# Performance work log

Hardware: AMD Instinct MI355X
Metric: run time of the kernel (lower is better)

Reference implementation:

```python
import jax, jax.numpy as jnp
import numpy as np

TAU = 2.0        # LIF membrane time constant
V_TH = 1.0       # spike threshold (spikingjelly default)
ALPHA = 4.0      # surrogate.Sigmoid default alpha
T_STEPS = 4
NUM_HEADS = 8


@jax.custom_vjp
def spike(x):
    # Heaviside(x) with sigmoid surrogate gradient (x = v - v_threshold)
    return (x >= 0.0).astype(x.dtype)

def _spike_fwd(x):
    return spike(x), x

def _spike_bwd(x, g):
    sg = jax.nn.sigmoid(ALPHA * x)
    return (g * ALPHA * sg * (1.0 - sg),)

spike.defvjp(_spike_fwd, _spike_bwd)


def multistep_lif(x_seq):
    """MultiStepLIFNode(tau=2, v_reset=0, detach_reset=True), x_seq: [T, ...]."""
    def step(v, x):
        v = v + (x - v) / TAU                     # decay_input=True charge
        s = spike(v - V_TH)
        v = v * (1.0 - jax.lax.stop_gradient(s))  # hard reset, detached
        return v, s
    _, s_seq = jax.lax.scan(step, jnp.zeros_like(x_seq[0]), x_seq)
    return s_seq


def setup_inputs() -> dict:
    key = jax.random.key(0)
    kx, kq, kk, kv = jax.random.split(key, 4)
    B, S, C = 2, 1024, 512
    scale = 1.0 / np.sqrt(C)
    return {
        "x": jax.random.normal(kx, (B, S, C), dtype=jnp.float32),
        "Wq": jax.random.normal(kq, (C, C), dtype=jnp.float32) * scale,
        "Wk": jax.random.normal(kk, (C, C), dtype=jnp.float32) * scale,
        "Wv": jax.random.normal(kv, (C, C), dtype=jnp.float32) * scale,
    }


def reference(x, Wq, Wk, Wv):
    B, S, C = x.shape
    H = NUM_HEADS
    hd = C // H
    # replicate input over T timesteps: [T, B, S, C]
    xt = jnp.broadcast_to(x[None], (T_STEPS, B, S, C))
    # nn.Linear applies x @ W.T
    q = multistep_lif(jnp.einsum('tbsc,dc->tbsd', xt, Wq))
    k = multistep_lif(jnp.einsum('tbsc,dc->tbsd', xt, Wk))
    v = multistep_lif(jnp.einsum('tbsc,dc->tbsd', xt, Wv))
    # [T, B, H, S, hd]
    q = q.reshape(T_STEPS, B, S, H, hd).transpose(0, 1, 3, 2, 4)
    k = k.reshape(T_STEPS, B, S, H, hd).transpose(0, 1, 3, 2, 4)
    v = v.reshape(T_STEPS, B, S, H, hd).transpose(0, 1, 3, 2, 4)
    scores = jnp.einsum('tbhqd,tbhkd->tbhqk', q, k) / jnp.sqrt(jnp.asarray(hd, x.dtype))
    scores = multistep_lif(scores)                  # LIF over T on [B,H,S,S]
    probs = jax.nn.softmax(scores, axis=-1)
    out = jnp.einsum('tbhqk,tbhkd->tbhqd', probs, v)  # [T,B,H,S,hd]
    out = out.transpose(0, 1, 3, 2, 4).reshape(T_STEPS, B, S, C)
    return out.mean(axis=0)
```

## Files before the change

### kernel.cpp

```cpp
#include <hip/hip_runtime.h>
#include <cstdint>

typedef unsigned long long u64;
typedef __attribute__((ext_vector_type(8))) _Float16 half8;
typedef __attribute__((ext_vector_type(4))) float f32x4;

#define RFL(x) __builtin_amdgcn_readfirstlane(x)

__device__ __forceinline__ void gload_lds16(const void* g, void* l) {
    __builtin_amdgcn_global_load_lds(
        (const __attribute__((address_space(1))) unsigned int*)g,
        (__attribute__((address_space(3))) unsigned int*)l, 16, 0, 0);
}


__global__ __launch_bounds__(256) void cvt_split16(
    const float* __restrict__ x,
    const float* __restrict__ Wq, const float* __restrict__ Wk,
    const float* __restrict__ Wv,
    _Float16* __restrict__ xh, _Float16* __restrict__ xl,
    _Float16* __restrict__ wh,
    unsigned* __restrict__ csbuf)
{
    const int bid = blockIdx.x;
    if (bid == 896) {
#pragma unroll
        for (int i = 0; i < 18; ++i) {
            const int idx = i * 256 + threadIdx.x;
            if (idx < 4608) csbuf[idx] = 0u;
        }
        return;
    }
    if (bid < 512) {
        const size_t j = (size_t)bid * 2048 + (size_t)threadIdx.x * 8;
        const float4 a = *(const float4*)(x + j);
        const float4 b = *(const float4*)(x + j + 4);
        const float va[8] = {a.x, a.y, a.z, a.w, b.x, b.y, b.z, b.w};
        half8 h8, l8;
#pragma unroll
        for (int i = 0; i < 8; ++i) {
            const _Float16 hi = (_Float16)va[i];
            h8[i] = hi;
            l8[i] = (_Float16)(va[i] - (float)hi);
        }
        *(half8*)(xh + j) = h8;
        *(half8*)(xl + j) = l8;
    } else {
        const size_t j = (size_t)(bid - 512) * 2048 + (size_t)threadIdx.x * 8;
        const int mat = (int)(j >> 18);
        const size_t off = j & 262143;
        const float* s = ((mat == 0) ? Wq : (mat == 1) ? Wk : Wv) + off;
        const float4 a = *(const float4*)s;
        const float4 b = *(const float4*)(s + 4);
        const float va[8] = {a.x, a.y, a.z, a.w, b.x, b.y, b.z, b.w};
        half8 h8;
#pragma unroll
        for (int i = 0; i < 8; ++i) h8[i] = (_Float16)va[i];
        *(half8*)(wh + j) = h8;
    }
}

#define AH_OFF 0
#define AL_OFF 8192
#define BH_OFF 16384
#define BUF_STRIDE 24576

__global__ __launch_bounds__(256) void gemm_mfma_lif_pack6(
    const _Float16* __restrict__ xh, const _Float16* __restrict__ xl,
    const _Float16* __restrict__ wh,
    u64* __restrict__ bits,
    unsigned* __restrict__ csbuf,
    u64* __restrict__ flags)
{
    __shared__ __align__(16) char smem[49152];

    const int tid  = threadIdx.x;
    const int lane = tid & 63;
    const int wv   = RFL(tid >> 6);
    const int byn = blockIdx.x;
    const int bx  = blockIdx.y;
    const int mat = byn >> 3, h = byn & 7;

    const int wm = wv >> 1, wn = wv & 1;
    const int lg = lane >> 4, lr = lane & 15;

    const int lrow8 = lane >> 3;
    const int koff  = ((lane & 7) ^ lrow8) * 8;

    f32x4 acc[2][2] = {{{0.f,0.f,0.f,0.f},{0.f,0.f,0.f,0.f}},
                       {{0.f,0.f,0.f,0.f},{0.f,0.f,0.f,0.f}}};

#define STAGE(buf, k0)                                                        \
    {                                                                         \
        const int base_ = (buf) * BUF_STRIDE;                                 \
        _Pragma("unroll")                                                     \
        for (int sp = 0; sp < 2; ++sp) {                                      \
            const int stripe = wv * 2 + sp;                                   \
            const int row = stripe * 8 + lrow8;                               \
            const size_t aoff = (size_t)(bx * 64 + row) * 512 + (k0) + koff;  \
            const size_t boff = (size_t)(byn * 64 + row) * 512 + (k0) + koff; \
            gload_lds16(xh + aoff, smem + base_ + AH_OFF + stripe * 1024);    \
            gload_lds16(xl + aoff, smem + base_ + AL_OFF + stripe * 1024);    \
            gload_lds16(wh + boff, smem + base_ + BH_OFF + stripe * 1024);    \
        }                                                                     \
    }

    STAGE(0, 0);
    __syncthreads();

    for (int it = 0; it < 8; ++it) {
        const int cur = it & 1;
        if (it < 7) STAGE(cur ^ 1, (it + 1) * 64);

        const int base = cur * BUF_STRIDE;
#pragma unroll
        for (int kk = 0; kk < 64; kk += 32) {
            const int slotb = (kk >> 3) + lg;
            half8 ah[2], al[2], bh2[2];
#pragma unroll
            for (int fm = 0; fm < 2; ++fm) {
                const int row = wm * 32 + fm * 16 + lr;
                const int off = base + row * 128 + ((slotb ^ (row & 7)) << 4);
                ah[fm] = *(const half8*)(smem + AH_OFF + off);
                al[fm] = *(const half8*)(smem + AL_OFF + off);
            }
#pragma unroll
            for (int fn = 0; fn < 2; ++fn) {
                const int row = wn * 32 + fn * 16 + lr;
                const int off = base + row * 128 + ((slotb ^ (row & 7)) << 4);
                bh2[fn] = *(const half8*)(smem + BH_OFF + off);
            }
#pragma unroll
            for (int fm = 0; fm < 2; ++fm)
#pragma unroll
                for (int fn = 0; fn < 2; ++fn) {
                    acc[fm][fn] = __builtin_amdgcn_mfma_f32_16x16x32_f16(
                        ah[fm], bh2[fn], acc[fm][fn], 0, 0, 0);
                    acc[fm][fn] = __builtin_amdgcn_mfma_f32_16x16x32_f16(
                        al[fm], bh2[fn], acc[fm][fn], 0, 0, 0);
                }
        }
        __syncthreads();
    }
#undef STAGE

    float* yl = (float*)smem;
#pragma unroll
    for (int fm = 0; fm < 2; ++fm)
#pragma unroll
        for (int fn = 0; fn < 2; ++fn)
#pragma unroll
            for (int reg = 0; reg < 4; ++reg) {
                const int m_loc = wm * 32 + fm * 16 + lg * 4 + reg;
                const int n_loc = wn * 32 + fn * 16 + lr;
                yl[m_loc * 65 + n_loc] = acc[fm][fn][reg];
            }
    __syncthreads();

    int pcnt[4] = {0, 0, 0, 0};
    u64 flagbits = 0;
    for (int r = 0; r < 16; ++r) {
        const int lrow = wv * 16 + r;
        const float y = yl[lrow * 65 + lane];
        float v = 0.f;
        int sp[4];
#pragma unroll
        for (int t = 0; t < 4; ++t) {
            v = v + (y - v) * 0.5f;
            const int s = (v - 1.0f >= 0.f) ? 1 : 0;
            v = s ? 0.f : v;
            sp[t] = s;
            pcnt[t] += s;
        }
        const int grow = bx * 64 + lrow;
        const int bb = grow >> 10;
        const int ss = grow & 1023;
        u64* dst = bits + (((size_t)(mat * 4) * 2 + bb) * 8 + h) * 1024 + ss;
        u64 mskarr[4];
#pragma unroll
        for (int t = 0; t < 4; ++t) {
            const u64 msk = __ballot(sp[t]);
            mskarr[t] = msk;
            if (lane == 0) dst[(size_t)t * (2 * 8 * 1024)] = msk;
        }
        if (mat == 0) {
            const int cc0 = (int)__popcll(mskarr[0]);
            const int cc1 = (int)__popcll(mskarr[1]);
            const int cc2 = (int)__popcll(mskarr[2]);
            const int cc3 = (int)__popcll(mskarr[3]);
            unsigned B = (unsigned)(cc0 << 2);
            unsigned mB = B;
            B = (B >> 1) + (unsigned)(cc1 << 2); mB = max(mB, B);
            B = (B >> 1) + (unsigned)(cc2 << 2); mB = max(mB, B);
            B = (B >> 1) + (unsigned)(cc3 << 2); mB = max(mB, B);
            if (mB >= 64u) flagbits |= (1ull << lrow);
        }
    }
    if (mat == 2) {
        const int bb = (bx * 64) >> 10;
        const int bh = bb * 8 + h;
#pragma unroll
        for (int t = 0; t < 4; ++t)
            atomicAdd(&csbuf[bh * 256 + t * 64 + lane], (unsigned)pcnt[t]);
    }
    if (mat == 0 && lane == 0 && flagbits) {
        const int bb = (bx * 64) >> 10;
        const int bh = bb * 8 + h;
        atomicOr(&flags[bh * 16 + (bx & 15)], flagbits);
    }
}

__global__ __launch_bounds__(256) void spike_attn10(
    const u64* __restrict__ bits,
    const unsigned* __restrict__ csbuf,
    const u64* __restrict__ flags,
    float* __restrict__ out)
{
    __shared__ u64 kb_s[4][1024];

    const int lane = threadIdx.x & 63;
    const int wave = RFL((int)(threadIdx.x >> 6));
    const int rt = blockIdx.x;
    const int h  = blockIdx.y;
    const int b  = blockIdx.z;

    const int bh = b * 8 + h;
    const u64* __restrict__ qb = bits + (size_t)bh * 1024;
    const u64* __restrict__ kb = bits + (size_t)(64 + bh) * 1024;
    const u64* __restrict__ vb = bits + (size_t)(128 + bh) * 1024;

    {
        const u64* __restrict__ srcT = kb + (size_t)wave * 16384;
#pragma unroll
        for (int i = 0; i < 8; ++i)
            gload_lds16(srcT + i * 128 + lane * 2, &kb_s[wave][i * 128]);
    }

    int cs[4];
#pragma unroll
    for (int t = 0; t < 4; ++t)
        cs[t] = (int)csbuf[bh * 256 + t * 64 + lane];
    const float base = (float)(cs[0] + cs[1] + cs[2] + cs[3]) * (1.0f / 4096.0f);

    const int s0 = rt * 16 + wave * 4;
    const u64 flagw = flags[bh * 16 + (s0 >> 6)];

    __syncthreads();

    const float E1 = 0.36787944117144233f;

#pragma unroll
    for (int r = 0; r < 4; ++r) {
        const int s = s0 + r;
        float o = base;
        if ((flagw >> (s & 63)) & 1ull) {
            const u64 q0 = qb[s];
            const u64 q1 = qb[16384 + s];
            const u64 q2 = qb[32768 + s];
            const u64 q3 = qb[49152 + s];
            int found = 0;
            for (int w = 0; w < 16; ++w) {
                const int ko = (w << 6) + lane;
                const int pc0 = (int)__popcll(kb_s[0][ko] & q0);
                const int pc1 = (int)__popcll(kb_s[1][ko] & q1);
                const int pc2 = (int)__popcll(kb_s[2][ko] & q2);
                const int pc3 = (int)__popcll(kb_s[3][ko] & q3);
                found = max(found, max(max(pc0, pc1), max(pc2, pc3)));
            }
            const u64 any = __ballot(found >= 9);
            if (any) {
                int msum[4] = {0, 0, 0, 0}, n11[4] = {0, 0, 0, 0};
                for (int w = 0; w < 16; ++w) {
                    const int ko = (w << 6) + lane;
                    const int pcs[4] = {
                        (int)__popcll(kb_s[0][ko] & q0),
                        (int)__popcll(kb_s[1][ko] & q1),
                        (int)__popcll(kb_s[2][ko] & q2),
                        (int)__popcll(kb_s[3][ko] & q3)};
                    unsigned u = 0;
#pragma unroll
                    for (int t = 0; t < 4; ++t) {
                        u = (u >> 1) + (unsigned)(pcs[t] << 2);
                        const int spk = (u >= 64u) ? 1 : 0;
                        const u64 msk = __ballot(spk);
                        u = spk ? 0u : u;
                        msum[t] += (int)__popcll(msk);
                        u64 m = msk;
                        while (m) {
                            const int j = (int)__builtin_ctzll(m);
                            m &= m - 1;
                            const u64 vw = vb[t * 16384 + (w << 6) + j];
                            n11[t] += (int)((vw >> lane) & 1ull);
                        }
                    }
                }
                o = 0.f;
#pragma unroll
                for (int t = 0; t < 4; ++t) {
                    const float mf = (float)msum[t];
                    const float Z  = mf + (1024.f - mf) * E1;
                    const float p1 = 1.0f / Z;
                    const float p0 = E1 / Z;
                    o += p0 * (float)cs[t] + (p1 - p0) * (float)n11[t];
                }
                o *= 0.25f;
            }
        }
        out[((size_t)b * 1024 + s) * 512 + (h << 6) + lane] = o;
    }
}

extern "C" void kernel_launch(void* const* d_in, const int* in_sizes, int n_in,
                              void* d_out, int out_size, void* d_ws, size_t ws_size,
                              hipStream_t stream) {
    const float* x  = (const float*)d_in[0];
    const float* Wq = (const float*)d_in[1];
    const float* Wk = (const float*)d_in[2];
    const float* Wv = (const float*)d_in[3];
    float* out = (float*)d_out;

    u64* bits = (u64*)d_ws;
    _Float16* xh = (_Float16*)((char*)d_ws + (2u << 20));
    _Float16* xl = xh + (size_t)2048 * 512;
    _Float16* wh = xl + (size_t)2048 * 512;
    unsigned* csbuf = (unsigned*)(wh + (size_t)1536 * 512);
    u64* flags = (u64*)(csbuf + 4096);

    cvt_split16<<<dim3(897), 256, 0, stream>>>(x, Wq, Wk, Wv, xh, xl, wh, csbuf);
    gemm_mfma_lif_pack6<<<dim3(24, 32), 256, 0, stream>>>(xh, xl, wh, bits, csbuf, flags);
    spike_attn10<<<dim3(64, 8, 2), 256, 0, stream>>>(bits, csbuf, flags, out);
}
```

Measured before the change: 32.75 us.

## Widen GEMM tile to cover two heads per block for A-operand reuse

The fused projection GEMM and LIF kernel now computes a 64x128 output tile spanning two heads instead of 64x64. A-operand loads (the xh and xl split halves) are reused across twice as many columns, and the block count halves. The epilogue loops over both heads for spike packing, counts and flags. In exchange, shared memory rises to 64KB and accumulators per thread double, which may reduce occupancy, and fewer blocks may leave CUs underused.

```diff
diff --git a/kernel.cpp b/kernel.cpp
--- a/kernel.cpp
+++ b/kernel.cpp
@@ -63,23 +63,25 @@
 #define AH_OFF 0
 #define AL_OFF 8192
 #define BH_OFF 16384
-#define BUF_STRIDE 24576
-
-__global__ __launch_bounds__(256) void gemm_mfma_lif_pack6(
+#define BUF_STRIDE 32768
+
+__global__ __launch_bounds__(256) void gemm_mfma_lif_pack8(
     const _Float16* __restrict__ xh, const _Float16* __restrict__ xl,
     const _Float16* __restrict__ wh,
     u64* __restrict__ bits,
     unsigned* __restrict__ csbuf,
     u64* __restrict__ flags)
 {
-    __shared__ __align__(16) char smem[49152];
+    __shared__ __align__(16) char smem[65536];
 
     const int tid  = threadIdx.x;
     const int lane = tid & 63;
     const int wv   = RFL(tid >> 6);
-    const int byn = blockIdx.x;
-    const int bx  = blockIdx.y;
-    const int mat = byn >> 3, h = byn & 7;
+    const int byn2 = blockIdx.x;
+    const int bx   = blockIdx.y;
+    const int mat = byn2 >> 2, hp = byn2 & 3;
+    const int h2  = hp * 2;
+    const int wrow0 = mat * 512 + hp * 128;
 
     const int wm = wv >> 1, wn = wv & 1;
     const int lg = lane >> 4, lr = lane & 15;
@@ -87,20 +89,28 @@
     const int lrow8 = lane >> 3;
     const int koff  = ((lane & 7) ^ lrow8) * 8;
 
-    f32x4 acc[2][2] = {{{0.f,0.f,0.f,0.f},{0.f,0.f,0.f,0.f}},
-                       {{0.f,0.f,0.f,0.f},{0.f,0.f,0.f,0.f}}};
+    f32x4 acc[2][4];
+#pragma unroll
+    for (int i = 0; i < 2; ++i)
+#pragma unroll
+        for (int j = 0; j < 4; ++j) acc[i][j] = (f32x4){0.f, 0.f, 0.f, 0.f};
 
 #define STAGE(buf, k0)                                                        \
     {                                                                         \
         const int base_ = (buf) * BUF_STRIDE;                                 \
         _Pragma("unroll")                                                     \
-        for (int sp = 0; sp < 2; ++sp) {                                      \
+        for (int sp = 0; sp < 2; ++sp) {          \
             const int stripe = wv * 2 + sp;                                   \
             const int row = stripe * 8 + lrow8;                               \
             const size_t aoff = (size_t)(bx * 64 + row) * 512 + (k0) + koff;  \
-            const size_t boff = (size_t)(byn * 64 + row) * 512 + (k0) + koff; \
             gload_lds16(xh + aoff, smem + base_ + AH_OFF + stripe * 1024);    \
             gload_lds16(xl + aoff, smem + base_ + AL_OFF + stripe * 1024);    \
+        }                                                                     \
+        _Pragma("unroll")                                                     \
+        for (int sq = 0; sq < 4; ++sq) {          \
+            const int stripe = wv * 4 + sq;                                   \
+            const int row = stripe * 8 + lrow8;                               \
+            const size_t boff = (size_t)(wrow0 + row) * 512 + (k0) + koff;    \
             gload_lds16(wh + boff, smem + base_ + BH_OFF + stripe * 1024);    \
         }                                                                     \
     }
@@ -116,7 +126,7 @@
 #pragma unroll
         for (int kk = 0; kk < 64; kk += 32) {
             const int slotb = (kk >> 3) + lg;
-            half8 ah[2], al[2], bh2[2];
+            half8 ah[2], al[2], bh2[4];
 #pragma unroll
             for (int fm = 0; fm < 2; ++fm) {
                 const int row = wm * 32 + fm * 16 + lr;
@@ -125,15 +135,15 @@
                 al[fm] = *(const half8*)(smem + AL_OFF + off);
             }
 #pragma unroll
-            for (int fn = 0; fn < 2; ++fn) {
-                const int row = wn * 32 + fn * 16 + lr;
+            for (int fn = 0; fn < 4; ++fn) {
+                const int row = wn * 64 + fn * 16 + lr;
                 const int off = base + row * 128 + ((slotb ^ (row & 7)) << 4);
                 bh2[fn] = *(const half8*)(smem + BH_OFF + off);
             }
 #pragma unroll
             for (int fm = 0; fm < 2; ++fm)
 #pragma unroll
-                for (int fn = 0; fn < 2; ++fn) {
+                for (int fn = 0; fn < 4; ++fn) {
                     acc[fm][fn] = __builtin_amdgcn_mfma_f32_16x16x32_f16(
                         ah[fm], bh2[fn], acc[fm][fn], 0, 0, 0);
                     acc[fm][fn] = __builtin_amdgcn_mfma_f32_16x16x32_f16(
@@ -148,65 +158,77 @@
 #pragma unroll
     for (int fm = 0; fm < 2; ++fm)
 #pragma unroll
-        for (int fn = 0; fn < 2; ++fn)
+        for (int fn = 0; fn < 4; ++fn)
 #pragma unroll
             for (int reg = 0; reg < 4; ++reg) {
                 const int m_loc = wm * 32 + fm * 16 + lg * 4 + reg;
-                const int n_loc = wn * 32 + fn * 16 + lr;
-                yl[m_loc * 65 + n_loc] = acc[fm][fn][reg];
+                const int n_loc = wn * 64 + fn * 16 + lr;
+                yl[m_loc * 130 + n_loc] = acc[fm][fn][reg];
             }
     __syncthreads();
 
-    int pcnt[4] = {0, 0, 0, 0};
-    u64 flagbits = 0;
+    int pcnt[2][4];
+#pragma unroll
+    for (int hh = 0; hh < 2; ++hh)
+#pragma unroll
+        for (int t = 0; t < 4; ++t) pcnt[hh][t] = 0;
+    u64 flagbits[2] = {0, 0};
+
     for (int r = 0; r < 16; ++r) {
         const int lrow = wv * 16 + r;
-        const float y = yl[lrow * 65 + lane];
-        float v = 0.f;
-        int sp[4];
-#pragma unroll
-        for (int t = 0; t < 4; ++t) {
-            v = v + (y - v) * 0.5f;
-            const int s = (v - 1.0f >= 0.f) ? 1 : 0;
-            v = s ? 0.f : v;
-            sp[t] = s;
-            pcnt[t] += s;
-        }
         const int grow = bx * 64 + lrow;
         const int bb = grow >> 10;
         const int ss = grow & 1023;
-        u64* dst = bits + (((size_t)(mat * 4) * 2 + bb) * 8 + h) * 1024 + ss;
-        u64 mskarr[4];
-#pragma unroll
-        for (int t = 0; t < 4; ++t) {
-            const u64 msk = __ballot(sp[t]);
-            mskarr[t] = msk;
-            if (lane == 0) dst[(size_t)t * (2 * 8 * 1024)] = msk;
-        }
-        if (mat == 0) {
-            const int cc0 = (int)__popcll(mskarr[0]);
-            const int cc1 = (int)__popcll(mskarr[1]);
-            const int cc2 = (int)__popcll(mskarr[2]);
-            const int cc3 = (int)__popcll(mskarr[3]);
-            unsigned B = (unsigned)(cc0 << 2);
-            unsigned mB = B;
-            B = (B >> 1) + (unsigned)(cc1 << 2); mB = max(mB, B);
-            B = (B >> 1) + (unsigned)(cc2 << 2); mB = max(mB, B);
-            B = (B >> 1) + (unsigned)(cc3 << 2); mB = max(mB, B);
-            if (mB >= 64u) flagbits |= (1ull << lrow);
-        }
-    }
+#pragma unroll
+        for (int hh = 0; hh < 2; ++hh) {
+            const float y = yl[lrow * 130 + hh * 64 + lane];
+            float v = 0.f;
+            int sp[4];
+#pragma unroll
+            for (int t = 0; t < 4; ++t) {
+                v = v + (y - v) * 0.5f;
+                const int s = (v - 1.0f >= 0.f) ? 1 : 0;
+                v = s ? 0.f : v;
+                sp[t] = s;
+                pcnt[hh][t] += s;
+            }
+            u64* dst = bits + (((size_t)(mat * 4) * 2 + bb) * 8 + (h2 + hh)) * 1024 + ss;
+            u64 mskarr[4];
+#pragma unroll
+            for (int t = 0; t < 4; ++t) {
+                const u64 msk = __ballot(sp[t]);
+                mskarr[t] = msk;
+                if (lane == 0) dst[(size_t)t * (2 * 8 * 1024)] = msk;
+            }
+            if (mat == 0) {
+                const int cc0 = (int)__popcll(mskarr[0]);
+                const int cc1 = (int)__popcll(mskarr[1]);
+                const int cc2 = (int)__popcll(mskarr[2]);
+                const int cc3 = (int)__popcll(mskarr[3]);
+                unsigned B = (unsigned)(cc0 << 2);
+                unsigned mB = B;
+                B = (B >> 1) + (unsigned)(cc1 << 2); mB = max(mB, B);
+                B = (B >> 1) + (unsigned)(cc2 << 2); mB = max(mB, B);
+                B = (B >> 1) + (unsigned)(cc3 << 2); mB = max(mB, B);
+                if (mB >= 64u) flagbits[hh] |= (1ull << lrow);
+            }
+        }
+    }
+    const int bb = (bx * 64) >> 10;
     if (mat == 2) {
-        const int bb = (bx * 64) >> 10;
-        const int bh = bb * 8 + h;
-#pragma unroll
-        for (int t = 0; t < 4; ++t)
-            atomicAdd(&csbuf[bh * 256 + t * 64 + lane], (unsigned)pcnt[t]);
-    }
-    if (mat == 0 && lane == 0 && flagbits) {
-        const int bb = (bx * 64) >> 10;
-        const int bh = bb * 8 + h;
-        atomicOr(&flags[bh * 16 + (bx & 15)], flagbits);
+#pragma unroll
+        for (int hh = 0; hh < 2; ++hh) {
+            const int bh = bb * 8 + h2 + hh;
+#pragma unroll
+            for (int t = 0; t < 4; ++t)
+                atomicAdd(&csbuf[bh * 256 + t * 64 + lane], (unsigned)pcnt[hh][t]);
+        }
+    }
+    if (mat == 0 && lane == 0) {
+#pragma unroll
+        for (int hh = 0; hh < 2; ++hh)
+            if (flagbits[hh])
+                atomicOr(&flags[(bb * 8 + h2 + hh) * 16 + (bx & 15)], flagbits[hh]);
     }
 }
 
@@ -327,6 +349,6 @@
     u64* flags = (u64*)(csbuf + 4096);
 
     cvt_split16<<<dim3(897), 256, 0, stream>>>(x, Wq, Wk, Wv, xh, xl, wh, csbuf);
-    gemm_mfma_lif_pack6<<<dim3(24, 32), 256, 0, stream>>>(xh, xl, wh, bits, csbuf, flags);
+    gemm_mfma_lif_pack8<<<dim3(12, 32), 256, 0, stream>>>(xh, xl, wh, bits, csbuf, flags);
     spike_attn10<<<dim3(64, 8, 2), 256, 0, stream>>>(bits, csbuf, flags, out);
 }
```

Result: slower. 35.24 us (+7.6%).
